# Kernel tuning notes

Hardware: AMD Instinct MI355X
Metric: run time of the kernel (lower is better)

Reference implementation:

```python
import jax, jax.numpy as jnp
import numpy as np

EPS = 1e-5  # torch LayerNorm default
N_BLOCKS = 8
N_NODES = 4096
BATCH = 4096


def setup_inputs() -> dict:
    key = jax.random.key(0)
    ks = jax.random.split(key, 4)
    scale = 1.0 / np.sqrt(N_NODES)  # keep activations sane through 8 GEMMs
    x = jax.random.normal(ks[0], (BATCH, N_NODES), dtype=jnp.float32)
    W = jax.random.normal(ks[1], (N_BLOCKS, N_NODES, N_NODES), dtype=jnp.float32) * scale
    b = jax.random.normal(ks[2], (N_BLOCKS, N_NODES), dtype=jnp.float32) * 0.01
    slope = jax.random.uniform(ks[3], (N_BLOCKS, N_NODES), dtype=jnp.float32)
    ln_g = jnp.ones((N_BLOCKS, N_NODES), dtype=jnp.float32)
    ln_b = jnp.zeros((N_BLOCKS, N_NODES), dtype=jnp.float32)
    return {"x": x, "ln_g": ln_g, "ln_b": ln_b, "W": W, "b": b, "slope": slope}


def _block(x, g, bt, Wi, bi, si):
    # LayerNorm over last dim (biased variance, eps inside sqrt) -> Linear -> per-feature LeakyReLU
    mu = jnp.mean(x, axis=-1, keepdims=True)
    var = jnp.mean(jnp.square(x - mu), axis=-1, keepdims=True)
    ln = (x - mu) * jax.lax.rsqrt(var + EPS) * g + bt
    y = jnp.einsum('bn,mn->bm', ln, Wi) + bi  # torch Linear: x @ W.T + b
    return jnp.where(y < 0, y * si, y)


def reference(x, ln_g, ln_b, W, b, slope):
    for i in range(N_BLOCKS):
        x = _block(x, ln_g[i], ln_b[i], W[i], b[i], slope[i])
    return x
```

## Files before the change

kernel.cpp:

```cpp
#include <hip/hip_runtime.h>
#include <hip/hip_bf16.h>

#define NNODES 4096
#define NBATCH 4096
#define NBLK 8
#define LN_EPS 1e-5f

typedef __attribute__((ext_vector_type(8))) short short8;
typedef __attribute__((ext_vector_type(4))) float f32x4;
typedef __attribute__((ext_vector_type(4))) unsigned short u16x4;
typedef unsigned short u16;

__device__ __forceinline__ u16 bf16_rn(float f) {
  unsigned int u = __builtin_bit_cast(unsigned int, f);
  u += 0x7fffu + ((u >> 16) & 1u);
  return (u16)(u >> 16);
}

__device__ __forceinline__ float bf16_to_f(u16 h) {
  unsigned int u = ((unsigned int)h) << 16;
  return __builtin_bit_cast(float, u);
}

__device__ __forceinline__ void load_lds16(const void* g, void* l) {
  __builtin_amdgcn_global_load_lds((const __attribute__((address_space(1))) void*)g,
                                   (__attribute__((address_space(3))) void*)l,
                                   16, 0, 0);
}

__global__ __launch_bounds__(256) void prep_kernel(const float* __restrict__ W,
                                                   u16* __restrict__ Wb,
                                                   const float* __restrict__ xin,
                                                   const float* __restrict__ g,
                                                   const float* __restrict__ bt,
                                                   u16* __restrict__ lnout) {
  __shared__ float sh[8];
  int t = threadIdx.x;
  if (blockIdx.x < 16384) {
    int idx = blockIdx.x * 256 + t;
    float4 v = ((const float4*)W)[idx];
    u16x4 o;
    o[0] = bf16_rn(v.x); o[1] = bf16_rn(v.y); o[2] = bf16_rn(v.z); o[3] = bf16_rn(v.w);
    ((u16x4*)Wb)[idx] = o;
    return;
  }
  int row = blockIdx.x - 16384;
  float f[16];
  float s = 0.f, ss = 0.f;
  const float4* xr = (const float4*)(xin + (size_t)row * NNODES);
#pragma unroll
  for (int q = 0; q < 4; ++q) {
    float4 v = xr[q * 256 + t];
    f[q * 4 + 0] = v.x; f[q * 4 + 1] = v.y; f[q * 4 + 2] = v.z; f[q * 4 + 3] = v.w;
    s  += v.x + v.y + v.z + v.w;
    ss += v.x * v.x + v.y * v.y + v.z * v.z + v.w * v.w;
  }
#pragma unroll
  for (int off = 32; off >= 1; off >>= 1) {
    s  += __shfl_xor(s, off, 64);
    ss += __shfl_xor(ss, off, 64);
  }
  int wid = t >> 6, lane = t & 63;
  if (lane == 0) { sh[wid] = s; sh[wid + 4] = ss; }
  __syncthreads();
  s  = sh[0] + sh[1] + sh[2] + sh[3];
  ss = sh[4] + sh[5] + sh[6] + sh[7];
  float mu  = s * (1.f / NNODES);
  float var = ss * (1.f / NNODES) - mu * mu;
  float rs  = rsqrtf(var + LN_EPS);
  u16x4* o = (u16x4*)(lnout + (size_t)row * NNODES);
  const float4* gv = (const float4*)g;
  const float4* bv = (const float4*)bt;
#pragma unroll
  for (int q = 0; q < 4; ++q) {
    int i = q * 256 + t;
    float4 gg = gv[i], bb = bv[i];
    u16x4 ov;
    ov[0] = bf16_rn((f[q * 4 + 0] - mu) * rs * gg.x + bb.x);
    ov[1] = bf16_rn((f[q * 4 + 1] - mu) * rs * gg.y + bb.y);
    ov[2] = bf16_rn((f[q * 4 + 2] - mu) * rs * gg.z + bb.z);
    ov[3] = bf16_rn((f[q * 4 + 3] - mu) * rs * gg.w + bb.w);
    o[i] = ov;
  }
}

__global__ __launch_bounds__(256) void ln_bf16_kernel(const u16* __restrict__ x,
                                                      const float* __restrict__ g,
                                                      const float* __restrict__ bt,
                                                      u16* __restrict__ out) {
  int row = blockIdx.x;
  int t = threadIdx.x;
  const u16* xr = x + (size_t)row * NNODES;
  float f[2][8];
  float s = 0.f, ss = 0.f;
#pragma unroll
  for (int q = 0; q < 2; ++q) {
    short8 v = *(const short8*)(xr + q * 2048 + t * 8);
#pragma unroll
    for (int j = 0; j < 8; ++j) {
      float fv = bf16_to_f((u16)v[j]);
      f[q][j] = fv;
      s += fv; ss += fv * fv;
    }
  }
#pragma unroll
  for (int off = 32; off >= 1; off >>= 1) {
    s  += __shfl_xor(s, off, 64);
    ss += __shfl_xor(ss, off, 64);
  }
  __shared__ float sh[8];
  int wid = t >> 6, lane = t & 63;
  if (lane == 0) { sh[wid] = s; sh[wid + 4] = ss; }
  __syncthreads();
  s  = sh[0] + sh[1] + sh[2] + sh[3];
  ss = sh[4] + sh[5] + sh[6] + sh[7];
  float mu  = s * (1.f / NNODES);
  float var = ss * (1.f / NNODES) - mu * mu;
  float rs  = rsqrtf(var + LN_EPS);
  const float4* gv = (const float4*)g;
  const float4* bv = (const float4*)bt;
#pragma unroll
  for (int q = 0; q < 2; ++q) {
    int base = q * 2048 + t * 8;
    float4 g0 = gv[base / 4], g1 = gv[base / 4 + 1];
    float4 b0 = bv[base / 4], b1 = bv[base / 4 + 1];
    short8 sv;
    sv[0] = (short)bf16_rn((f[q][0] - mu) * rs * g0.x + b0.x);
    sv[1] = (short)bf16_rn((f[q][1] - mu) * rs * g0.y + b0.y);
    sv[2] = (short)bf16_rn((f[q][2] - mu) * rs * g0.z + b0.z);
    sv[3] = (short)bf16_rn((f[q][3] - mu) * rs * g0.w + b0.w);
    sv[4] = (short)bf16_rn((f[q][4] - mu) * rs * g1.x + b1.x);
    sv[5] = (short)bf16_rn((f[q][5] - mu) * rs * g1.y + b1.y);
    sv[6] = (short)bf16_rn((f[q][6] - mu) * rs * g1.z + b1.z);
    sv[7] = (short)bf16_rn((f[q][7] - mu) * rs * g1.w + b1.w);
    *(short8*)(out + (size_t)row * NNODES + base) = sv;
  }
}


#define VMC(N) asm volatile("s_waitcnt vmcnt(" #N ")" ::: "memory")

#define STAGE_A(T, H)                                                          \
  { load_lds16(Asrc0 + (size_t)((H) * 128) * Kdim + (T) * 64,                  \
               ldsA + ((T) & 1) * 16384 + (H) * 8192 + tid * 8);               \
    load_lds16(Asrc0 + (size_t)((H) * 128 + 64) * Kdim + (T) * 64,             \
               ldsA + ((T) & 1) * 16384 + (H) * 8192 + 4096 + tid * 8); }

#define STAGE_B(T, H)                                                          \
  { load_lds16(Bsrc0 + (size_t)((H) * 128) * Kdim + (T) * 64,                  \
               ldsB + ((T) & 1) * 16384 + (H) * 8192 + tid * 8);               \
    load_lds16(Bsrc0 + (size_t)((H) * 128 + 64) * Kdim + (T) * 64,             \
               ldsB + ((T) & 1) * 16384 + (H) * 8192 + 4096 + tid * 8); }

#define CVSTORE(SRC, CIDX)                                                     \
  { u16x4 o_;                                                                  \
    o_[0] = bf16_rn(SRC[0]); o_[1] = bf16_rn(SRC[1]);                          \
    o_[2] = bf16_rn(SRC[2]); o_[3] = bf16_rn(SRC[3]);                          \
    *(u16x4*)(Wnd + cvoff + (size_t)(CIDX) * 2048) = o_; }

#define CONVP2                                                                 \
  { if (CONVON && t >= 1 && t <= 16) {                                         \
      __builtin_amdgcn_sched_barrier(0);                                       \
      CVSTORE(cvA, 2 * (t - 1))                                                \
      CVSTORE(cvB, 2 * (t - 1) + 1)                                            \
    }                                                                          \
    if (CONVON && t < 16) {                                                    \
      const float* cpa_ = Wns + cvoff + (size_t)(2 * t) * 2048;                \
      const float* cpb_ = Wns + cvoff + (size_t)(2 * t + 1) * 2048;            \
      asm volatile("global_load_dwordx4 %0, %2, off\n\t"                       \
                   "global_load_dwordx4 %1, %3, off"                           \
                   : "=&v"(cvA), "=&v"(cvB) : "v"(cpa_), "v"(cpb_)             \
                   : "memory");                                                \
    } }

#define VMP3                                                                   \
  { if (CONVON) {                                                              \
      if (t == 0 || t == 16) { VMC(4); }                                       \
      else if (t < 16)       { VMC(6); }                                       \
      else                   { VMC(2); }                                       \
    } else { VMC(2); } }

#define PH1(KT, MH, NH, STAGE_STMT, VM_STMT)                                   \
  {                                                                            \
    const u16* Ab = ldsA + ((KT) & 1) * 16384 + aBase + (MH) * 4096;           \
    const u16* Bb = ldsB + ((KT) & 1) * 16384 + bBase + (NH) * 2048;           \
    if ((NH) == 0) {                                                           \
      _Pragma("unroll") for (int mi = 0; mi < 4; ++mi) {                       \
        afr[mi][0] = *(const short8*)(Ab + mi * 1024 + gk0);                   \
        afr[mi][1] = *(const short8*)(Ab + mi * 1024 + gk1);                   \
      }                                                                        \
    }                                                                          \
    if ((MH) == 0) {                                                           \
      _Pragma("unroll") for (int ni = 0; ni < 2; ++ni) {                       \
        bfr[NH][ni][0] = *(const short8*)(Bb + ni * 1024 + gk0);               \
        bfr[NH][ni][1] = *(const short8*)(Bb + ni * 1024 + gk1);               \
      }                                                                        \
    }                                                                          \
    STAGE_STMT;                                                                \
    if ((NH) == 0 && (MH) == 0)                                                \
      asm volatile("s_waitcnt lgkmcnt(8)" ::: "memory");                       \
    VM_STMT;                                                                   \
    __builtin_amdgcn_s_barrier();                                              \
    asm volatile("s_waitcnt lgkmcnt(0)" ::: "memory");                         \
    __builtin_amdgcn_sched_barrier(0);                                         \
    __builtin_amdgcn_s_setprio(1);                                             \
    _Pragma("unroll") for (int mi = 0; mi < 4; ++mi)                           \
      _Pragma("unroll") for (int ni = 0; ni < 2; ++ni) {                       \
        acc[(MH) * 4 + mi][(NH) * 2 + ni] =                                    \
          __builtin_amdgcn_mfma_f32_16x16x32_bf16(afr[mi][0], bfr[NH][ni][0],  \
            acc[(MH) * 4 + mi][(NH) * 2 + ni], 0, 0, 0);                       \
        acc[(MH) * 4 + mi][(NH) * 2 + ni] =                                    \
          __builtin_amdgcn_mfma_f32_16x16x32_bf16(afr[mi][1], bfr[NH][ni][1],  \
            acc[(MH) * 4 + mi][(NH) * 2 + ni], 0, 0, 0);                       \
      }                                                                        \
    __builtin_amdgcn_s_setprio(0);                                             \
  }

template <bool OUTF32, bool CONVON>
__global__ __launch_bounds__(512, 2) void gemm256_kernel(const u16* __restrict__ A,
                                                         const u16* __restrict__ B,
                                                         const float* __restrict__ bias,
                                                         const float* __restrict__ slope,
                                                         void* __restrict__ Cv,
                                                         const float* __restrict__ Wns,
                                                         u16* __restrict__ Wnd) {
  constexpr int Kdim = NNODES;
  __shared__ u16 lds[65536];
  u16* ldsA = lds;
  u16* ldsB = lds + 32768;

  const int tid  = threadIdx.x;
  const int lane = tid & 63;
  const int wid  = tid >> 6;
  const int wr   = wid >> 2;
  const int wc   = wid & 3;

  int bid = blockIdx.x;
  int swz = (bid & 7) * 32 + (bid >> 3);
  const int brow = (swz >> 4) * 256;
  const int bcol = (swz & 15) * 256;

  const int srow = tid >> 3;
  const int sg   = ((tid & 7) ^ (srow & 7)) * 8;
  const u16* Asrc0 = A + (size_t)(brow + srow) * Kdim + sg;
  const u16* Bsrc0 = B + (size_t)(bcol + srow) * Kdim + sg;

  const int r16 = lane & 15, kq = lane >> 4;
  const int g0  = kq ^ (r16 & 7);
  const int gk0 = g0 * 8, gk1 = (g0 ^ 4) * 8;
  const int aBase = wr * 8192 + r16 * 64;
  const int bBase = (wc >> 1) * 8192 + ((wc & 1) * 64 + r16) * 64;

  const size_t cvoff = (size_t)bid * 65536 + tid * 4;
  f32x4 cvA, cvB;

  f32x4 acc[8][4] = {};
  short8 afr[4][2], bfr[2][2][2];

  STAGE_B(0, 0) STAGE_B(0, 1) STAGE_A(0, 0) STAGE_A(0, 1) STAGE_B(1, 0) STAGE_B(1, 1)
  VMC(4);
  __builtin_amdgcn_s_barrier();

  for (int t = 0; t < 31; ++t) {
    const int T = 2 * t;
    PH1(T,     0, 0, STAGE_A(T + 1, 0), ;)
    PH1(T,     0, 1, STAGE_A(T + 1, 1), ;)
    PH1(T,     1, 0, CONVP2,            ;)
    PH1(T,     1, 1, STAGE_B(T + 2, 0), VMP3)
    PH1(T + 1, 0, 0, STAGE_B(T + 2, 1), ;)
    PH1(T + 1, 0, 1, STAGE_A(T + 2, 0), ;)
    PH1(T + 1, 1, 0, STAGE_A(T + 2, 1), ;)
    PH1(T + 1, 1, 1, { STAGE_B(T + 3, 0) STAGE_B(T + 3, 1) }, VMC(4))
  }
  PH1(62, 0, 0, STAGE_A(63, 0), ;)
  PH1(62, 0, 1, STAGE_A(63, 1), ;)
  PH1(62, 1, 0, ;, ;)
  PH1(62, 1, 1, ;, VMC(0))
  PH1(63, 0, 0, ;, ;)
  PH1(63, 0, 1, ;, ;)
  PH1(63, 1, 0, ;, ;)
  PH1(63, 1, 1, ;, ;)

  const int crow0 = brow + wr * 128 + (lane >> 4) * 4;
  const int ccol0 = bcol + wc * 64 + r16;
#pragma unroll
  for (int n = 0; n < 4; ++n) {
    int col = ccol0 + n * 16;
    float bv = bias[col], sv = slope[col];
#pragma unroll
    for (int m = 0; m < 8; ++m) {
      int row0 = crow0 + m * 16;
#pragma unroll
      for (int r = 0; r < 4; ++r) {
        float vv = acc[m][n][r] + bv;
        vv = vv < 0.f ? vv * sv : vv;
        if constexpr (OUTF32) {
          ((float*)Cv)[(size_t)(row0 + r) * NNODES + col] = vv;
        } else {
          ((u16*)Cv)[(size_t)(row0 + r) * NNODES + col] = bf16_rn(vv);
        }
      }
    }
  }
}

extern "C" void kernel_launch(void* const* d_in, const int* in_sizes, int n_in,
                              void* d_out, int out_size, void* d_ws, size_t ws_size,
                              hipStream_t stream) {
  const float* x     = (const float*)d_in[0];
  const float* ln_g  = (const float*)d_in[1];
  const float* ln_b  = (const float*)d_in[2];
  const float* W     = (const float*)d_in[3];
  const float* b     = (const float*)d_in[4];
  const float* slope = (const float*)d_in[5];
  float* out = (float*)d_out;

  char* ws = (char*)d_ws;
  u16* Wbuf0 = (u16*)ws;
  u16* Wbuf1 = (u16*)(ws + (size_t)32 * 1024 * 1024);
  u16* lnbuf = (u16*)(ws + (size_t)64 * 1024 * 1024);
  u16* ybuf  = (u16*)(ws + (size_t)96 * 1024 * 1024);

  const size_t WN = (size_t)NNODES * NNODES;

  for (int i = 0; i < NBLK; ++i) {
    u16* Wc = (i & 1) ? Wbuf1 : Wbuf0;
    u16* Wn = (i & 1) ? Wbuf0 : Wbuf1;
    if (i == 0)
      prep_kernel<<<dim3(16384 + NBATCH), dim3(256), 0, stream>>>(
          W, Wbuf0, x, ln_g, ln_b, lnbuf);
    else
      ln_bf16_kernel<<<dim3(NBATCH), dim3(256), 0, stream>>>(
          ybuf, ln_g + (size_t)i * NNODES, ln_b + (size_t)i * NNODES, lnbuf);

    if (i == NBLK - 1)
      gemm256_kernel<true, false><<<dim3(256), dim3(512), 0, stream>>>(
          lnbuf, Wc, b + (size_t)i * NNODES, slope + (size_t)i * NNODES,
          (void*)out, nullptr, nullptr);
    else
      gemm256_kernel<false, true><<<dim3(256), dim3(512), 0, stream>>>(
          lnbuf, Wc, b + (size_t)i * NNODES, slope + (size_t)i * NNODES,
          (void*)ybuf, W + WN * (i + 1), Wn);
  }
}
```

Before: 1.049 ms.

## Fuse all GEMM and LayerNorm stages into one persistent kernel with grid barriers

Replaces the per-block sequence of LayerNorm and GEMM kernel launches with a single persistent kernel of 256 workgroups. The stages are separated by a software grid barrier built on global atomics. LayerNorm is now done inside the same kernel, one wave per row, to remove launch gaps and tail effects between the 15 launches. It risks deadlock if all 256 workgroups are not co-resident, adds barrier spin cost, and may fall back to using the output buffer for the sync counters.

```diff
diff --git a/kernel.cpp b/kernel.cpp
--- a/kernel.cpp
+++ b/kernel.cpp
@@ -5,6 +5,7 @@
 #define NBATCH 4096
 #define NBLK 8
 #define LN_EPS 1e-5f
+#define NGRID 256u
 
 typedef __attribute__((ext_vector_type(8))) short short8;
 typedef __attribute__((ext_vector_type(4))) float f32x4;
@@ -26,6 +27,24 @@
   __builtin_amdgcn_global_load_lds((const __attribute__((address_space(1))) void*)g,
                                    (__attribute__((address_space(3))) void*)l,
                                    16, 0, 0);
+}
+
+__device__ __forceinline__ void grid_barrier(unsigned* cnt, unsigned* gen) {
+  __syncthreads();
+  if (threadIdx.x == 0) {
+    __threadfence();
+    unsigned g = __hip_atomic_load(gen, __ATOMIC_RELAXED, __HIP_MEMORY_SCOPE_AGENT);
+    unsigned a = __hip_atomic_fetch_add(cnt, 1u, __ATOMIC_ACQ_REL, __HIP_MEMORY_SCOPE_AGENT);
+    if (a == NGRID - 1u) {
+      __hip_atomic_store(cnt, 0u, __ATOMIC_RELAXED, __HIP_MEMORY_SCOPE_AGENT);
+      __hip_atomic_fetch_add(gen, 1u, __ATOMIC_RELEASE, __HIP_MEMORY_SCOPE_AGENT);
+    } else {
+      while (__hip_atomic_load(gen, __ATOMIC_ACQUIRE, __HIP_MEMORY_SCOPE_AGENT) == g)
+        __builtin_amdgcn_s_sleep(2);
+    }
+    __threadfence();
+  }
+  __syncthreads();
 }
 
 __global__ __launch_bounds__(256) void prep_kernel(const float* __restrict__ W,
@@ -84,59 +103,53 @@
   }
 }
 
-__global__ __launch_bounds__(256) void ln_bf16_kernel(const u16* __restrict__ x,
-                                                      const float* __restrict__ g,
-                                                      const float* __restrict__ bt,
-                                                      u16* __restrict__ out) {
-  int row = blockIdx.x;
-  int t = threadIdx.x;
-  const u16* xr = x + (size_t)row * NNODES;
-  float f[2][8];
-  float s = 0.f, ss = 0.f;
-#pragma unroll
-  for (int q = 0; q < 2; ++q) {
-    short8 v = *(const short8*)(xr + q * 2048 + t * 8);
-#pragma unroll
-    for (int j = 0; j < 8; ++j) {
-      float fv = bf16_to_f((u16)v[j]);
-      f[q][j] = fv;
-      s += fv; ss += fv * fv;
-    }
-  }
-#pragma unroll
-  for (int off = 32; off >= 1; off >>= 1) {
-    s  += __shfl_xor(s, off, 64);
-    ss += __shfl_xor(ss, off, 64);
-  }
-  __shared__ float sh[8];
-  int wid = t >> 6, lane = t & 63;
-  if (lane == 0) { sh[wid] = s; sh[wid + 4] = ss; }
-  __syncthreads();
-  s  = sh[0] + sh[1] + sh[2] + sh[3];
-  ss = sh[4] + sh[5] + sh[6] + sh[7];
-  float mu  = s * (1.f / NNODES);
-  float var = ss * (1.f / NNODES) - mu * mu;
-  float rs  = rsqrtf(var + LN_EPS);
-  const float4* gv = (const float4*)g;
-  const float4* bv = (const float4*)bt;
-#pragma unroll
-  for (int q = 0; q < 2; ++q) {
-    int base = q * 2048 + t * 8;
-    float4 g0 = gv[base / 4], g1 = gv[base / 4 + 1];
-    float4 b0 = bv[base / 4], b1 = bv[base / 4 + 1];
-    short8 sv;
-    sv[0] = (short)bf16_rn((f[q][0] - mu) * rs * g0.x + b0.x);
-    sv[1] = (short)bf16_rn((f[q][1] - mu) * rs * g0.y + b0.y);
-    sv[2] = (short)bf16_rn((f[q][2] - mu) * rs * g0.z + b0.z);
-    sv[3] = (short)bf16_rn((f[q][3] - mu) * rs * g0.w + b0.w);
-    sv[4] = (short)bf16_rn((f[q][4] - mu) * rs * g1.x + b1.x);
-    sv[5] = (short)bf16_rn((f[q][5] - mu) * rs * g1.y + b1.y);
-    sv[6] = (short)bf16_rn((f[q][6] - mu) * rs * g1.z + b1.z);
-    sv[7] = (short)bf16_rn((f[q][7] - mu) * rs * g1.w + b1.w);
-    *(short8*)(out + (size_t)row * NNODES + base) = sv;
-  }
-}
-
+__device__ __forceinline__ void ln_pass(const u16* __restrict__ y,
+                                        const float* __restrict__ g,
+                                        const float* __restrict__ bt,
+                                        u16* __restrict__ lnout,
+                                        int bid, int wid, int lane) {
+#pragma unroll
+  for (int rr = 0; rr < 2; ++rr) {
+    int row = bid * 16 + wid * 2 + rr;
+    const u16* xr = y + (size_t)row * NNODES + lane * 8;
+    short8 v[8];
+    float s = 0.f, ss = 0.f;
+#pragma unroll
+    for (int q = 0; q < 8; ++q) {
+      v[q] = *(const short8*)(xr + q * 512);
+#pragma unroll
+      for (int j = 0; j < 8; ++j) {
+        float f = bf16_to_f((u16)v[q][j]);
+        s += f; ss += f * f;
+      }
+    }
+#pragma unroll
+    for (int off = 32; off >= 1; off >>= 1) {
+      s  += __shfl_xor(s, off, 64);
+      ss += __shfl_xor(ss, off, 64);
+    }
+    float mu  = s * (1.f / NNODES);
+    float var = ss * (1.f / NNODES) - mu * mu;
+    float rs  = rsqrtf(var + LN_EPS);
+    u16* o = lnout + (size_t)row * NNODES + lane * 8;
+#pragma unroll
+    for (int q = 0; q < 8; ++q) {
+      int base = lane * 8 + q * 512;
+      float4 g0 = *(const float4*)(g + base), g1 = *(const float4*)(g + base + 4);
+      float4 b0 = *(const float4*)(bt + base), b1 = *(const float4*)(bt + base + 4);
+      short8 sv;
+      sv[0] = (short)bf16_rn((bf16_to_f((u16)v[q][0]) - mu) * rs * g0.x + b0.x);
+      sv[1] = (short)bf16_rn((bf16_to_f((u16)v[q][1]) - mu) * rs * g0.y + b0.y);
+      sv[2] = (short)bf16_rn((bf16_to_f((u16)v[q][2]) - mu) * rs * g0.z + b0.z);
+      sv[3] = (short)bf16_rn((bf16_to_f((u16)v[q][3]) - mu) * rs * g0.w + b0.w);
+      sv[4] = (short)bf16_rn((bf16_to_f((u16)v[q][4]) - mu) * rs * g1.x + b1.x);
+      sv[5] = (short)bf16_rn((bf16_to_f((u16)v[q][5]) - mu) * rs * g1.y + b1.y);
+      sv[6] = (short)bf16_rn((bf16_to_f((u16)v[q][6]) - mu) * rs * g1.z + b1.z);
+      sv[7] = (short)bf16_rn((bf16_to_f((u16)v[q][7]) - mu) * rs * g1.w + b1.w);
+      *(short8*)(o + q * 512) = sv;
+    }
+  }
+}
 
 #define VMC(N) asm volatile("s_waitcnt vmcnt(" #N ")" ::: "memory")
 
@@ -217,15 +230,15 @@
   }
 
 template <bool OUTF32, bool CONVON>
-__global__ __launch_bounds__(512, 2) void gemm256_kernel(const u16* __restrict__ A,
-                                                         const u16* __restrict__ B,
-                                                         const float* __restrict__ bias,
-                                                         const float* __restrict__ slope,
-                                                         void* __restrict__ Cv,
-                                                         const float* __restrict__ Wns,
-                                                         u16* __restrict__ Wnd) {
+__device__ __forceinline__ void gemm_body(const u16* __restrict__ A,
+                                          const u16* __restrict__ B,
+                                          const float* __restrict__ bias,
+                                          const float* __restrict__ slope,
+                                          void* __restrict__ Cv,
+                                          const float* __restrict__ Wns,
+                                          u16* __restrict__ Wnd,
+                                          u16* lds) {
   constexpr int Kdim = NNODES;
-  __shared__ u16 lds[65536];
   u16* ldsA = lds;
   u16* ldsB = lds + 32768;
 
@@ -304,6 +317,42 @@
   }
 }
 
+__global__ __launch_bounds__(512, 2) void mega_kernel(const float* __restrict__ W,
+                                                      const float* __restrict__ ln_g,
+                                                      const float* __restrict__ ln_b,
+                                                      const float* __restrict__ b,
+                                                      const float* __restrict__ slope,
+                                                      u16* __restrict__ Wbuf0,
+                                                      u16* __restrict__ Wbuf1,
+                                                      u16* __restrict__ lnbuf,
+                                                      u16* __restrict__ ybuf,
+                                                      float* __restrict__ out,
+                                                      unsigned* cnt, unsigned* gen) {
+  __shared__ u16 lds[65536];
+  const size_t WN = (size_t)NNODES * NNODES;
+  const int bid = blockIdx.x;
+  const int wid = threadIdx.x >> 6;
+  const int lane = threadIdx.x & 63;
+
+  gemm_body<false, true>(lnbuf, Wbuf0, b, slope, (void*)ybuf, W + WN, Wbuf1, lds);
+  grid_barrier(cnt, gen);
+
+  for (int i = 1; i < 7; ++i) {
+    ln_pass(ybuf, ln_g + (size_t)i * NNODES, ln_b + (size_t)i * NNODES, lnbuf, bid, wid, lane);
+    grid_barrier(cnt, gen);
+    const u16* Wc = (i & 1) ? Wbuf1 : Wbuf0;
+    u16* Wn = (i & 1) ? Wbuf0 : Wbuf1;
+    gemm_body<false, true>(lnbuf, Wc, b + (size_t)i * NNODES, slope + (size_t)i * NNODES,
+                           (void*)ybuf, W + WN * (i + 1), Wn, lds);
+    grid_barrier(cnt, gen);
+  }
+
+  ln_pass(ybuf, ln_g + (size_t)7 * NNODES, ln_b + (size_t)7 * NNODES, lnbuf, bid, wid, lane);
+  grid_barrier(cnt, gen);
+  gemm_body<true, false>(lnbuf, Wbuf1, b + (size_t)7 * NNODES, slope + (size_t)7 * NNODES,
+                         (void*)out, nullptr, nullptr, lds);
+}
+
 extern "C" void kernel_launch(void* const* d_in, const int* in_sizes, int n_in,
                               void* d_out, int out_size, void* d_ws, size_t ws_size,
                               hipStream_t stream) {
@@ -321,25 +370,12 @@
   u16* lnbuf = (u16*)(ws + (size_t)64 * 1024 * 1024);
   u16* ybuf  = (u16*)(ws + (size_t)96 * 1024 * 1024);
 
-  const size_t WN = (size_t)NNODES * NNODES;
-
-  for (int i = 0; i < NBLK; ++i) {
-    u16* Wc = (i & 1) ? Wbuf1 : Wbuf0;
-    u16* Wn = (i & 1) ? Wbuf0 : Wbuf1;
-    if (i == 0)
-      prep_kernel<<<dim3(16384 + NBATCH), dim3(256), 0, stream>>>(
-          W, Wbuf0, x, ln_g, ln_b, lnbuf);
-    else
-      ln_bf16_kernel<<<dim3(NBATCH), dim3(256), 0, stream>>>(
-          ybuf, ln_g + (size_t)i * NNODES, ln_b + (size_t)i * NNODES, lnbuf);
-
-    if (i == NBLK - 1)
-      gemm256_kernel<true, false><<<dim3(256), dim3(512), 0, stream>>>(
-          lnbuf, Wc, b + (size_t)i * NNODES, slope + (size_t)i * NNODES,
-          (void*)out, nullptr, nullptr);
-    else
-      gemm256_kernel<false, true><<<dim3(256), dim3(512), 0, stream>>>(
-          lnbuf, Wc, b + (size_t)i * NNODES, slope + (size_t)i * NNODES,
-          (void*)ybuf, W + WN * (i + 1), Wn);
-  }
-}
+  const size_t used = (size_t)128 * 1024 * 1024;
+  unsigned* sync = (ws_size >= used + 64) ? (unsigned*)(ws + used) : (unsigned*)d_out;
+  hipMemsetAsync((void*)sync, 0, 8, stream);
+
+  prep_kernel<<<dim3(16384 + NBATCH), dim3(256), 0, stream>>>(W, Wbuf0, x, ln_g, ln_b, lnbuf);
+  mega_kernel<<<dim3(NGRID), dim3(512), 0, stream>>>(W, ln_g, ln_b, b, slope,
+                                                     Wbuf0, Wbuf1, lnbuf, ybuf, out,
+                                                     sync, sync + 1);
+}
```

New measurement: 1.997 ms. +90.4%, slower.

## Restructure GEMM main loop into two phases per K-tile with whole-tile staging

Applied to the files above, without the earlier changes.

The main loop changes from four sub-phases per K-tile (each loading part of A/B fragments and staging half-tiles) to two phases per K-tile. All A and B fragments are loaded from LDS up front, and the whole next tile is staged in one go. This halves the number of barriers per tile and simplifies the vmcnt waits to full drains. In exchange it raises register pressure (afr doubles) and makes global-load prefetch coarser, which may reduce overlap of memory latency with MFMA work.

```diff
diff --git a/kernel.cpp b/kernel.cpp
--- a/kernel.cpp
+++ b/kernel.cpp
@@ -152,13 +152,15 @@
     load_lds16(Bsrc0 + (size_t)((H) * 128 + 64) * Kdim + (T) * 64,             \
                ldsB + ((T) & 1) * 16384 + (H) * 8192 + 4096 + tid * 8); }
 
+#define STAGE_TILE(T) { STAGE_A(T, 0) STAGE_A(T, 1) STAGE_B(T, 0) STAGE_B(T, 1) }
+
 #define CVSTORE(SRC, CIDX)                                                     \
   { u16x4 o_;                                                                  \
     o_[0] = bf16_rn(SRC[0]); o_[1] = bf16_rn(SRC[1]);                          \
     o_[2] = bf16_rn(SRC[2]); o_[3] = bf16_rn(SRC[3]);                          \
     *(u16x4*)(Wnd + cvoff + (size_t)(CIDX) * 2048) = o_; }
 
-#define CONVP2                                                                 \
+#define CONVP1                                                                 \
   { if (CONVON && t >= 1 && t <= 16) {                                         \
       __builtin_amdgcn_sched_barrier(0);                                       \
       CVSTORE(cvA, 2 * (t - 1))                                                \
@@ -173,45 +175,55 @@
                    : "memory");                                                \
     } }
 
-#define VMP3                                                                   \
+#define VMP1                                                                   \
   { if (CONVON) {                                                              \
-      if (t == 0 || t == 16) { VMC(4); }                                       \
-      else if (t < 16)       { VMC(6); }                                       \
-      else                   { VMC(2); }                                       \
-    } else { VMC(2); } }
-
-#define PH1(KT, MH, NH, STAGE_STMT, VM_STMT)                                   \
+      if (t == 0 || t == 16) { VMC(2); }                                       \
+      else if (t < 16)       { VMC(4); }                                       \
+      else                   { VMC(0); }                                       \
+    } else { VMC(0); } }
+
+#define PH_R(KT, STAGE_STMT)                                                   \
   {                                                                            \
-    const u16* Ab = ldsA + ((KT) & 1) * 16384 + aBase + (MH) * 4096;           \
-    const u16* Bb = ldsB + ((KT) & 1) * 16384 + bBase + (NH) * 2048;           \
-    if ((NH) == 0) {                                                           \
-      _Pragma("unroll") for (int mi = 0; mi < 4; ++mi) {                       \
-        afr[mi][0] = *(const short8*)(Ab + mi * 1024 + gk0);                   \
-        afr[mi][1] = *(const short8*)(Ab + mi * 1024 + gk1);                   \
+    const u16* Ab = ldsA + ((KT) & 1) * 16384 + aBase;                         \
+    const u16* Bb = ldsB + ((KT) & 1) * 16384 + bBase;                         \
+    _Pragma("unroll") for (int mi = 0; mi < 8; ++mi) {                         \
+      afr[mi][0] = *(const short8*)(Ab + mi * 1024 + gk0);                     \
+      afr[mi][1] = *(const short8*)(Ab + mi * 1024 + gk1);                     \
+    }                                                                          \
+    _Pragma("unroll") for (int nh = 0; nh < 2; ++nh)                           \
+      _Pragma("unroll") for (int ni = 0; ni < 2; ++ni) {                       \
+        bfr[nh][ni][0] = *(const short8*)(Bb + nh * 2048 + ni * 1024 + gk0);   \
+        bfr[nh][ni][1] = *(const short8*)(Bb + nh * 2048 + ni * 1024 + gk1);   \
       }                                                                        \
-    }                                                                          \
-    if ((MH) == 0) {                                                           \
+    STAGE_STMT;                                                                \
+    __builtin_amdgcn_s_barrier();                                              \
+    asm volatile("s_waitcnt lgkmcnt(0)" ::: "memory");                         \
+    __builtin_amdgcn_sched_barrier(0);                                         \
+    __builtin_amdgcn_s_setprio(1);                                             \
+    _Pragma("unroll") for (int mi = 0; mi < 8; ++mi)                           \
       _Pragma("unroll") for (int ni = 0; ni < 2; ++ni) {                       \
-        bfr[NH][ni][0] = *(const short8*)(Bb + ni * 1024 + gk0);               \
-        bfr[NH][ni][1] = *(const short8*)(Bb + ni * 1024 + gk1);               \
+        acc[mi][ni] = __builtin_amdgcn_mfma_f32_16x16x32_bf16(                 \
+            afr[mi][0], bfr[0][ni][0], acc[mi][ni], 0, 0, 0);                  \
+        acc[mi][ni] = __builtin_amdgcn_mfma_f32_16x16x32_bf16(                 \
+            afr[mi][1], bfr[0][ni][1], acc[mi][ni], 0, 0, 0);                  \
       }                                                                        \
-    }                                                                          \
-    STAGE_STMT;                                                                \
-    if ((NH) == 0 && (MH) == 0)                                                \
-      asm volatile("s_waitcnt lgkmcnt(8)" ::: "memory");                       \
+    __builtin_amdgcn_s_setprio(0);                                             \
+  }
+
+#define PH_N(CONV_STMT, VM_STMT)                                               \
+  {                                                                            \
+    CONV_STMT;                                                                 \
     VM_STMT;                                                                   \
     __builtin_amdgcn_s_barrier();                                              \
     asm volatile("s_waitcnt lgkmcnt(0)" ::: "memory");                         \
     __builtin_amdgcn_sched_barrier(0);                                         \
     __builtin_amdgcn_s_setprio(1);                                             \
-    _Pragma("unroll") for (int mi = 0; mi < 4; ++mi)                           \
+    _Pragma("unroll") for (int mi = 0; mi < 8; ++mi)                           \
       _Pragma("unroll") for (int ni = 0; ni < 2; ++ni) {                       \
-        acc[(MH) * 4 + mi][(NH) * 2 + ni] =                                    \
-          __builtin_amdgcn_mfma_f32_16x16x32_bf16(afr[mi][0], bfr[NH][ni][0],  \
-            acc[(MH) * 4 + mi][(NH) * 2 + ni], 0, 0, 0);                       \
-        acc[(MH) * 4 + mi][(NH) * 2 + ni] =                                    \
-          __builtin_amdgcn_mfma_f32_16x16x32_bf16(afr[mi][1], bfr[NH][ni][1],  \
-            acc[(MH) * 4 + mi][(NH) * 2 + ni], 0, 0, 0);                       \
+        acc[mi][2 + ni] = __builtin_amdgcn_mfma_f32_16x16x32_bf16(             \
+            afr[mi][0], bfr[1][ni][0], acc[mi][2 + ni], 0, 0, 0);              \
+        acc[mi][2 + ni] = __builtin_amdgcn_mfma_f32_16x16x32_bf16(             \
+            afr[mi][1], bfr[1][ni][1], acc[mi][2 + ni], 0, 0, 0);              \
       }                                                                        \
     __builtin_amdgcn_s_setprio(0);                                             \
   }
@@ -255,31 +267,23 @@
   f32x4 cvA, cvB;
 
   f32x4 acc[8][4] = {};
-  short8 afr[4][2], bfr[2][2][2];
-
-  STAGE_B(0, 0) STAGE_B(0, 1) STAGE_A(0, 0) STAGE_A(0, 1) STAGE_B(1, 0) STAGE_B(1, 1)
-  VMC(4);
+  short8 afr[8][2], bfr[2][2][2];
+
+  STAGE_TILE(0)
+  VMC(0);
   __builtin_amdgcn_s_barrier();
 
   for (int t = 0; t < 31; ++t) {
     const int T = 2 * t;
-    PH1(T,     0, 0, STAGE_A(T + 1, 0), ;)
-    PH1(T,     0, 1, STAGE_A(T + 1, 1), ;)
-    PH1(T,     1, 0, CONVP2,            ;)
-    PH1(T,     1, 1, STAGE_B(T + 2, 0), VMP3)
-    PH1(T + 1, 0, 0, STAGE_B(T + 2, 1), ;)
-    PH1(T + 1, 0, 1, STAGE_A(T + 2, 0), ;)
-    PH1(T + 1, 1, 0, STAGE_A(T + 2, 1), ;)
-    PH1(T + 1, 1, 1, { STAGE_B(T + 3, 0) STAGE_B(T + 3, 1) }, VMC(4))
-  }
-  PH1(62, 0, 0, STAGE_A(63, 0), ;)
-  PH1(62, 0, 1, STAGE_A(63, 1), ;)
-  PH1(62, 1, 0, ;, ;)
-  PH1(62, 1, 1, ;, VMC(0))
-  PH1(63, 0, 0, ;, ;)
-  PH1(63, 0, 1, ;, ;)
-  PH1(63, 1, 0, ;, ;)
-  PH1(63, 1, 1, ;, ;)
+    PH_R(T,     STAGE_TILE(T + 1))
+    PH_N(CONVP1, VMP1)
+    PH_R(T + 1, STAGE_TILE(T + 2))
+    PH_N(;, VMC(0))
+  }
+  PH_R(62, STAGE_TILE(63))
+  PH_N(;, VMC(0))
+  PH_R(63, ;)
+  PH_N(;, ;)
 
   const int crow0 = brow + wr * 128 + (lane >> 4) * 4;
   const int ccol0 = bcol + wc * 64 + r16;
```

Result: slower. 1.092 ms (+4.0%).
